# Kernel tuning notes

Hardware: AMD Instinct MI355X
Metric: run time of the kernel (lower is better)

Reference implementation:

```python
import math
import jax, jax.numpy as jnp
import numpy as np

NUM_HEADS = 32
NUM_KV_HEADS = 8
HEAD_SIZE = 128
FEATURE_DIM = 64
SEQ_LEN = 2048
WINDOW_SIZE = 64
EPS = 1e-12
MASK_VALUE = -100000000.0


def _make_masks(n: int, w: int):
    # block-diagonal ones(w,w) tiles, plus the rolled (sub-diagonal) tiles
    m = math.ceil(n / w)
    mask = np.kron(np.eye(m), np.ones((w, w)))
    mask = mask + np.roll(mask, -w, axis=-1)
    mask = mask[:n, :n]
    mask_window = np.tril(mask).astype(bool)[None, None]          # [1,1,n,n]
    mask_linear = np.tril(1.0 - mask).astype(bool)[None, None]    # [1,1,n,n]
    return jnp.asarray(mask_window), jnp.asarray(mask_linear)


def _feature_map(w, x):
    # f(x) = clamp(cat(softmax(xW), softmax(-xW)), min=eps)
    z = jnp.einsum('hdf,bhld->bhlf', w, x)
    return jnp.clip(
        jnp.concatenate([jax.nn.softmax(z, axis=-1), jax.nn.softmax(-z, axis=-1)], axis=-1),
        EPS, None)


def setup_inputs() -> dict:
    key = jax.random.key(0)
    ks = jax.random.split(key, 6)
    return {
        'query': jax.random.normal(ks[0], (SEQ_LEN, NUM_HEADS * HEAD_SIZE), dtype=jnp.float32),
        'key': jax.random.normal(ks[1], (SEQ_LEN, NUM_KV_HEADS * HEAD_SIZE), dtype=jnp.float32),
        'value': jax.random.normal(ks[2], (SEQ_LEN, NUM_KV_HEADS * HEAD_SIZE), dtype=jnp.float32),
        'fmap_q_w': 0.02 * jax.random.normal(ks[3], (NUM_HEADS, HEAD_SIZE, FEATURE_DIM), dtype=jnp.float32),
        'fmap_k_w': 0.02 * jax.random.normal(ks[4], (NUM_HEADS, HEAD_SIZE, FEATURE_DIM), dtype=jnp.float32),
        'window_factors': jax.random.normal(ks[5], (1, NUM_HEADS, 1, 1), dtype=jnp.float32),
    }


def reference(query, key, value, fmap_q_w, fmap_k_w, window_factors):
    T = query.shape[0]
    q = query.reshape(T, NUM_HEADS, HEAD_SIZE)
    k = key.reshape(T, NUM_KV_HEADS, HEAD_SIZE)
    v = value.reshape(T, NUM_KV_HEADS, HEAD_SIZE)
    rep = NUM_HEADS // NUM_KV_HEADS
    k = jnp.repeat(k, rep, axis=1)
    v = jnp.repeat(v, rep, axis=1)
    # [T,H,D] -> [1,H,T,D]
    q = jnp.moveaxis(q, 0, -2)[None]
    k = jnp.moveaxis(k, 0, -2)[None]
    v = jnp.moveaxis(v, 0, -2)[None]

    f_q = _feature_map(fmap_q_w, q)  # [1,H,T,2F]
    f_k = _feature_map(fmap_k_w, k)
    wf = jax.nn.sigmoid(window_factors)

    mask_window, mask_linear = _make_masks(SEQ_LEN, WINDOW_SIZE)
    mask_window = mask_window[:, :, :T, :T]
    mask_linear = mask_linear[:, :, :T, :T]

    # sliding-window softmax term
    a_sm = jnp.einsum('bhmd,bhnd->bhmn', q, k) * (HEAD_SIZE ** -0.5)
    a_sm = jnp.where(mask_window, a_sm, MASK_VALUE)
    a_sm_max = jnp.max(a_sm, axis=-1, keepdims=True)
    a_sm = wf * jnp.exp(a_sm - a_sm_max)
    sum_sm = jnp.sum(a_sm, axis=-1, keepdims=True)

    # linear feature-map term (linear_factor = 1)
    a_ln = jnp.einsum('bhmd,bhnd->bhmn', f_q, f_k)
    a_ln = jnp.where(mask_linear, a_ln, 0.0)
    sum_ln = jnp.sum(a_ln, axis=-1, keepdims=True)

    y = jnp.einsum('bhmn,bhnd->bhmd', a_sm + a_ln, v)
    return y / (sum_sm + sum_ln)
```

## Files before the change

### kernel.cpp

```cpp
#include <hip/hip_runtime.h>
#include <math.h>

#define T_SEQ 2048
#define NH    32
#define NKV   8
#define HS    128
#define FD    64
#define NBLK  32
#define SCAN_NB 30
#define EPSF  1e-12f
#define LDP   136
#define STP   129

typedef unsigned short u16;
typedef __bf16 bf16x8 __attribute__((ext_vector_type(8)));
typedef float  f32x4  __attribute__((ext_vector_type(4)));

__device__ __forceinline__ u16 f2b(float f) {
  unsigned u = __builtin_bit_cast(unsigned, f);
  return (u16)((u + 0x7fffu + ((u >> 16) & 1u)) >> 16);
}

#define FKT_OFF 0
#define ST_OFF  16777216
#define VT_OFF  54525952
#define WT_OFF  58720256
#define KB_OFF  59768832

__global__ __launch_bounds__(256) void k_pre(
    const float* __restrict__ wq, const float* __restrict__ wk,
    const float* __restrict__ vg,
    u16* __restrict__ WT, u16* __restrict__ VT)
{
  __shared__ float sB[128 * 68];
  const int bx = blockIdx.x, tid = threadIdx.x;

  if (bx < 64) {
    const int h = bx >> 1, isk = bx & 1;
    const float* src = (isk ? wk : wq) + (size_t)h * HS * FD;
    for (int idx = tid * 4; idx < 8192; idx += 1024) {
      int r = idx >> 6, c = idx & 63;
      *(float4*)(sB + r * 68 + c) = *(const float4*)(src + idx);
    }
    __syncthreads();
    u16* dst = WT + ((size_t)(isk * NH + h)) * 8192;
    for (int i = 0; i < 8; ++i) {
      int ch = tid + i * 256;
      int f = ch >> 5, d4 = (ch & 31) * 4;
      ushort4 u;
      u.x = f2b(sB[(d4 + 0) * 68 + f]);
      u.y = f2b(sB[(d4 + 1) * 68 + f]);
      u.z = f2b(sB[(d4 + 2) * 68 + f]);
      u.w = f2b(sB[(d4 + 3) * 68 + f]);
      *(ushort4*)(dst + f * 128 + d4) = u;
    }
  } else {
    const int idx2 = bx - 64;
    const int b = idx2 & 31, kvh = idx2 >> 5;
    float* sV = sB;
    for (int idx = tid * 4; idx < 8192; idx += 1024) {
      int r = idx >> 7, c = idx & 127;
      *(float4*)(sV + r * 129 + c) = *(const float4*)(vg + (size_t)(b * 64 + r) * (NKV * HS) + kvh * HS + c);
    }
    __syncthreads();
    const int lane = tid & 63, w = tid >> 6;
#pragma unroll
    for (int i = 0; i < 32; ++i) {
      int d = w * 32 + i;
      VT[((size_t)(kvh * 128 + d)) * T_SEQ + b * 64 + lane] = f2b(sV[lane * 129 + d]);
    }
  }
}

__global__ __launch_bounds__(256) void k_fmap(
    const float* __restrict__ kg, const u16* __restrict__ WT,
    u16* __restrict__ FKT, u16* __restrict__ KBB)
{
  __shared__ __align__(16) u16 smem[2 * 64 * 136];
  u16* sX = smem;
  u16* sW = smem + 64 * 136;
  const int lt = blockIdx.x, h = blockIdx.y;
  const int tid = threadIdx.x, lane = tid & 63, w = tid >> 6;
  const int quad = lane >> 4, txn = lane & 15;

  const float* xbase = kg + (h >> 2) * HS;
  const int    xstr  = NKV * HS;
  for (int idx = tid * 4; idx < 8192; idx += 1024) {
    int r = idx >> 7, c = idx & 127;
    float4 v4 = *(const float4*)(xbase + (size_t)(lt * 64 + r) * xstr + c);
    ushort4 u; u.x = f2b(v4.x); u.y = f2b(v4.y); u.z = f2b(v4.z); u.w = f2b(v4.w);
    *(ushort4*)(sX + r * 136 + c) = u;
  }
  const u16* wt = WT + ((size_t)(NH + h)) * 8192;
  for (int i = 0; i < 4; ++i) {
    int ch = tid + i * 256;
    int row = ch >> 4, d8 = (ch & 15) * 8;
    *(uint4*)(sW + row * 136 + d8) = *(const uint4*)(wt + row * 128 + d8);
  }
  __syncthreads();

  if ((h & 3) == 0) {
    u16* ob = KBB + ((size_t)((h >> 2) * NBLK + lt)) * 8192;
    for (int i = 0; i < 4; ++i) {
      int ch = tid + i * 256;
      int row = ch >> 4, d8 = (ch & 15) * 8;
      *(uint4*)(ob + row * 128 + d8) = *(const uint4*)(sX + row * 136 + d8);
    }
  }

  const int arow = w * 16 + txn;
  const f32x4 vzero = {0.f, 0.f, 0.f, 0.f};
  f32x4 zt[4] = {vzero, vzero, vzero, vzero};
#pragma unroll
  for (int ks = 0; ks < 4; ++ks) {
    bf16x8 a = *(const bf16x8*)(sX + arow * 136 + ks * 32 + quad * 8);
#pragma unroll
    for (int nt = 0; nt < 4; ++nt) {
      bf16x8 bb = *(const bf16x8*)(sW + (nt * 16 + txn) * 136 + ks * 32 + quad * 8);
      zt[nt] = __builtin_amdgcn_mfma_f32_16x16x32_bf16(a, bb, zt[nt], 0, 0, 0);
    }
  }

  float E1[4][4], E2[4][4];
#pragma unroll
  for (int r = 0; r < 4; ++r) {
    float zv[4];
    float mx = -1e30f, mn = 1e30f;
#pragma unroll
    for (int nt = 0; nt < 4; ++nt) {
      zv[nt] = zt[nt][r];
      mx = fmaxf(mx, zv[nt]); mn = fminf(mn, zv[nt]);
    }
#pragma unroll
    for (int o = 1; o < 16; o <<= 1) {
      mx = fmaxf(mx, __shfl_xor(mx, o));
      mn = fminf(mn, __shfl_xor(mn, o));
    }
    float e1[4], e2[4], s1 = 0.f, s2 = 0.f;
#pragma unroll
    for (int nt = 0; nt < 4; ++nt) {
      e1[nt] = __expf(zv[nt] - mx); s1 += e1[nt];
      e2[nt] = __expf(mn - zv[nt]); s2 += e2[nt];
    }
#pragma unroll
    for (int o = 1; o < 16; o <<= 1) { s1 += __shfl_xor(s1, o); s2 += __shfl_xor(s2, o); }
    float r1 = 1.f / s1, r2 = 1.f / s2;
#pragma unroll
    for (int nt = 0; nt < 4; ++nt) {
      E1[r][nt] = fmaxf(e1[nt] * r1, EPSF);
      E2[r][nt] = fmaxf(e2[nt] * r2, EPSF);
    }
  }

  __syncthreads();

#pragma unroll
  for (int r = 0; r < 4; ++r) {
    int j = w * 16 + quad * 4 + r;
#pragma unroll
    for (int nt = 0; nt < 4; ++nt) {
      sX[(nt * 16 + txn) * 68 + j]        = f2b(E1[r][nt]);
      sX[(nt * 16 + txn + 64) * 68 + j]   = f2b(E2[r][nt]);
    }
  }
  __syncthreads();
  u16* ob = FKT + (size_t)h * 128 * T_SEQ + lt * 64;
  for (int i = 0; i < 8; ++i) {
    int ch = tid + i * 256;
    int row = ch >> 4, j4 = (ch & 15) * 4;
    *(ushort4*)(ob + (size_t)row * T_SEQ + j4) = *(const ushort4*)(sX + row * 68 + j4);
  }
}

__global__ __launch_bounds__(256) void k_scan(
    const u16* __restrict__ FKT, const u16* __restrict__ VT, u16* __restrict__ ST)
{
  __shared__ __align__(16) u16 sVT[16 * 72];
  __shared__ __align__(16) u16 sFK[64 * 72];
  const int L = blockIdx.x + 8 * blockIdx.y + 16 * blockIdx.z;
  const int xcd = L & 7, j = L >> 3;
  const int hsub = j & 3, fh = (j >> 2) & 1, dc = j >> 3;
  const int h = xcd * 4 + hsub;
  const int tid = threadIdx.x, lane = tid & 63, w = tid >> 6;
  const int quad = lane >> 4, txn = lane & 15;
  const bool doz = (dc == 0);

  bf16x8 vone;
#pragma unroll
  for (int jj = 0; jj < 8; ++jj) vone[jj] = (__bf16)1.0f;

  const u16* vbase = VT + ((size_t)((h >> 2) * 128 + dc * 16)) * T_SEQ;
  const u16* fbase = FKT + ((size_t)(h * 128 + fh * 64)) * T_SEQ;

  const int srow = tid >> 4, sj4 = (tid & 15) * 4;
  ushort4 rv, rf[4];
  rv = *(const ushort4*)(vbase + (size_t)srow * T_SEQ + sj4);
#pragma unroll
  for (int i = 0; i < 4; ++i) {
    int ch = tid + i * 256;
    int fr = ch >> 4, fj4 = (ch & 15) * 4;
    rf[i] = *(const ushort4*)(fbase + (size_t)fr * T_SEQ + fj4);
  }

  const f32x4 vzero = {0.f, 0.f, 0.f, 0.f};
  f32x4 acc = vzero, zacc = vzero;

  for (int b = 0; b < SCAN_NB; ++b) {
    __syncthreads();
    *(ushort4*)(sVT + srow * 72 + sj4) = rv;
#pragma unroll
    for (int i = 0; i < 4; ++i) {
      int ch = tid + i * 256;
      int fr = ch >> 4, fj4 = (ch & 15) * 4;
      *(ushort4*)(sFK + fr * 72 + fj4) = rf[i];
    }
    __syncthreads();
    if (b + 1 < SCAN_NB) {
      rv = *(const ushort4*)(vbase + (size_t)srow * T_SEQ + (b + 1) * 64 + sj4);
#pragma unroll
      for (int i = 0; i < 4; ++i) {
        int ch = tid + i * 256;
        int fr = ch >> 4, fj4 = (ch & 15) * 4;
        rf[i] = *(const ushort4*)(fbase + (size_t)fr * T_SEQ + (b + 1) * 64 + fj4);
      }
    }
#pragma unroll
    for (int ks = 0; ks < 2; ++ks) {
      bf16x8 a  = *(const bf16x8*)(sVT + txn * 72 + ks * 32 + quad * 8);
      bf16x8 bb = *(const bf16x8*)(sFK + (w * 16 + txn) * 72 + ks * 32 + quad * 8);
      acc = __builtin_amdgcn_mfma_f32_16x16x32_bf16(a, bb, acc, 0, 0, 0);
      if (doz) zacc = __builtin_amdgcn_mfma_f32_16x16x32_bf16(vone, bb, zacc, 0, 0, 0);
    }
    u16* Sb = ST + (((size_t)(h * NBLK + b)) * STP + dc * 16) * 128 + fh * 64;
#pragma unroll
    for (int r = 0; r < 4; ++r)
      Sb[(quad * 4 + r) * 128 + w * 16 + txn] = f2b(acc[r]);
    if (doz && quad == 0)
      ST[(((size_t)(h * NBLK + b)) * STP + 128) * 128 + fh * 64 + w * 16 + txn] = f2b(zacc[0]);
  }
}

__global__ __launch_bounds__(512, 6) void k_main(
    const float* __restrict__ qg, const u16* __restrict__ KBB,
    const u16* __restrict__ WT, const u16* __restrict__ ST,
    const u16* __restrict__ VT, const float* __restrict__ wfac,
    float* __restrict__ out)
{
  __shared__ __align__(16) u16 RA[64 * LDP];
  __shared__ __align__(16) u16 RB[64 * LDP];
  __shared__ __align__(16) u16 sz[128];
  __shared__ float sred[256];
  const int L = blockIdx.x + 32 * blockIdx.y;
  const int xcd = L & 7, jj = L >> 3;
  const int hsub = jj & 3, B = jj >> 2;
  const int h = xcd * 4 + hsub;
  const int tid = threadIdx.x;
  const int lane = tid & 63, w = tid >> 6;
  const int wq_ = w & 3, wt = w >> 2;
  const int quad = lane >> 4, txn = lane & 15;
  const int arow = wq_ * 16 + txn;
  const int koff = quad * 8;

  const f32x4 vzero = {0.f, 0.f, 0.f, 0.f};
  f32x4 y[4];
#pragma unroll
  for (int t = 0; t < 4; ++t) y[t] = vzero;
  float sln[4] = {0.f, 0.f, 0.f, 0.f};
  const bf16x8 bzero = {0, 0, 0, 0, 0, 0, 0, 0};

  const int kb0 = (B >= 1) ? B - 1 : 0;
  const u16* ktB = KBB + ((size_t)((h >> 2) * NBLK + B)) * 8192;
  const u16* ktP = KBB + ((size_t)((h >> 2) * NBLK + kb0)) * 8192;
  const u16* vts = VT  + (size_t)((h >> 2) * 128) * T_SEQ;
  const u16* wqt = WT  + (size_t)h * 8192;
  const u16* ssrc = ST + ((size_t)(h * NBLK + (B >= 2 ? B - 2 : 0))) * (STP * 128);

  auto stage_full = [&](const u16* __restrict__ src) {
#pragma unroll
    for (int i = 0; i < 2; ++i) {
      int idx = tid * 8 + i * 4096, rr = idx >> 7, c = idx & 127;
      *(uint4*)(RB + rr * LDP + c) = *(const uint4*)(src + idx);
    }
  };
  auto stage_qk = [&](int p) {
#pragma unroll
    for (int i = 0; i < 2; ++i) {
      int idx = tid * 8 + i * 4096, rr = idx >> 7, c = idx & 127;
      const u16* src = (rr < 32) ? (ktB + (p * 32 + rr) * 128)
                                 : (ktP + (p * 32 + rr - 32) * 128);
      *(uint4*)(RB + rr * LDP + c) = *(const uint4*)(src + c);
    }
  };
  auto stage_v = [&](int p) {
#pragma unroll
    for (int i = 0; i < 2; ++i) {
      int idx = tid * 8 + i * 4096, rr = idx >> 7, c = idx & 127;
      int d = (rr < 32) ? (p * 32 + rr) : (64 + p * 32 + rr - 32);
      int key = (c < 64) ? (kb0 * 64 + c) : (B * 64 + (c - 64));
      *(uint4*)(RB + rr * LDP + c) = *(const uint4*)(vts + (size_t)d * T_SEQ + key);
    }
  };
  auto stage_s = [&](int p) {
#pragma unroll
    for (int i = 0; i < 2; ++i) {
      int idx = tid * 8 + i * 4096, rr = idx >> 7, c = idx & 127;
      int d = (rr < 32) ? (p * 32 + rr) : (64 + p * 32 + rr - 32);
      *(uint4*)(RB + rr * LDP + c) = *(const uint4*)(ssrc + d * 128 + c);
    }
  };

#pragma unroll
  for (int i = 0; i < 4; ++i) {
    int idx = tid * 4 + i * 2048;
    int r = idx >> 7, c = idx & 127;
    float4 v4 = *(const float4*)(qg + (size_t)(B * 64 + r) * (NH * HS) + h * HS + c);
    ushort4 u; u.x = f2b(v4.x); u.y = f2b(v4.y); u.z = f2b(v4.z); u.w = f2b(v4.w);
    *(ushort4*)(RA + r * LDP + c) = u;
  }
  if (B >= 2) stage_full(wqt);
  __syncthreads();

  f32x4 zt[4] = {vzero, vzero, vzero, vzero};
  if (B >= 2) {
#pragma unroll
    for (int ks = 0; ks < 4; ++ks) {
      bf16x8 a = *(const bf16x8*)(RA + arow * LDP + ks * 32 + koff);
#pragma unroll
      for (int nt = 0; nt < 4; ++nt) {
        bf16x8 bb = *(const bf16x8*)(RB + (nt * 16 + txn) * LDP + ks * 32 + koff);
        zt[nt] = __builtin_amdgcn_mfma_f32_16x16x32_bf16(a, bb, zt[nt], 0, 0, 0);
      }
    }
  }
  __syncthreads();
  stage_qk(0);

  unsigned Epk[4][4];
  if (B >= 2) {
#pragma unroll
    for (int r = 0; r < 4; ++r) {
      float zv[4];
      float mx = -1e30f, mn = 1e30f;
#pragma unroll
      for (int nt = 0; nt < 4; ++nt) {
        zv[nt] = zt[nt][r];
        mx = fmaxf(mx, zv[nt]); mn = fminf(mn, zv[nt]);
      }
#pragma unroll
      for (int o = 1; o < 16; o <<= 1) {
        mx = fmaxf(mx, __shfl_xor(mx, o));
        mn = fminf(mn, __shfl_xor(mn, o));
      }
      float e1[4], e2[4], s1 = 0.f, s2 = 0.f;
#pragma unroll
      for (int nt = 0; nt < 4; ++nt) {
        e1[nt] = __expf(zv[nt] - mx); s1 += e1[nt];
        e2[nt] = __expf(mn - zv[nt]); s2 += e2[nt];
      }
#pragma unroll
      for (int o = 1; o < 16; o <<= 1) { s1 += __shfl_xor(s1, o); s2 += __shfl_xor(s2, o); }
      float r1 = 1.f / s1, r2 = 1.f / s2;
#pragma unroll
      for (int nt = 0; nt < 4; ++nt) {
        unsigned lo = f2b(fmaxf(e1[nt] * r1, EPSF));
        unsigned hi = f2b(fmaxf(e2[nt] * r2, EPSF));
        Epk[r][nt] = lo | (hi << 16);
      }
    }
  }
  __syncthreads();

  f32x4 s[4];
#pragma unroll
  for (int t = 0; t < 4; ++t) s[t] = vzero;
#pragma unroll
  for (int ks = 0; ks < 4; ++ks) {
    bf16x8 a = *(const bf16x8*)(RA + arow * LDP + ks * 32 + koff);
#pragma unroll
    for (int tl = 0; tl < 2; ++tl) {
      if (wt == 0 && B == 0) continue;
      int row = (wt ? 0 : 32) + tl * 16 + txn;
      bf16x8 bb = *(const bf16x8*)(RB + row * LDP + ks * 32 + koff);
      s[tl] = __builtin_amdgcn_mfma_f32_16x16x32_bf16(a, bb, s[tl], 0, 0, 0);
    }
  }
  __syncthreads();
  stage_qk(1);
  __syncthreads();
#pragma unroll
  for (int ks = 0; ks < 4; ++ks) {
    bf16x8 a = *(const bf16x8*)(RA + arow * LDP + ks * 32 + koff);
#pragma unroll
    for (int tl = 0; tl < 2; ++tl) {
      if (wt == 0 && B == 0) continue;
      int row = (wt ? 0 : 32) + tl * 16 + txn;
      bf16x8 bb = *(const bf16x8*)(RB + row * LDP + ks * 32 + koff);
      s[2 + tl] = __builtin_amdgcn_mfma_f32_16x16x32_bf16(a, bb, s[2 + tl], 0, 0, 0);
    }
  }

  float wf = wfac[h];
  wf = 1.f / (1.f + __expf(-wf));
  const float scale = 0.08838834764831845f;
  float mh[4];
#pragma unroll
  for (int r = 0; r < 4; ++r) {
    const int irow = wq_ * 16 + quad * 4 + r;
    float m = -1e30f;
#pragma unroll
    for (int sl = 0; sl < 4; ++sl) {
      float x = s[sl][r] * scale;
      bool msk = wt ? (sl * 16 + txn > irow) : (B == 0);
      x = msk ? -1e30f : x;
      s[sl][r] = x;
      m = fmaxf(m, x);
    }
#pragma unroll
    for (int o = 1; o < 16; o <<= 1) m = fmaxf(m, __shfl_xor(m, o));
    mh[r] = m;
  }
  if (txn == 0) {
#pragma unroll
    for (int r = 0; r < 4; ++r) sred[wt * 64 + wq_ * 16 + quad * 4 + r] = mh[r];
  }
  __syncthreads();

  float ssum[4];
#pragma unroll
  for (int r = 0; r < 4; ++r) {
    const int irow = wq_ * 16 + quad * 4 + r;
    float m = fmaxf(mh[r], sred[(wt ^ 1) * 64 + wq_ * 16 + quad * 4 + r]);
    float ss = 0.f;
#pragma unroll
    for (int sl = 0; sl < 4; ++sl) {
      float e = (s[sl][r] > -1e29f) ? wf * __expf(s[sl][r] - m) : 0.f;
      ss += e;
      RA[irow * LDP + wt * 64 + sl * 16 + txn] = f2b(e);
    }
#pragma unroll
    for (int o = 1; o < 16; o <<= 1) ss += __shfl_xor(ss, o);
    ssum[r] = ss;
  }
  if (txn == 0) {
#pragma unroll
    for (int r = 0; r < 4; ++r) sred[128 + wt * 64 + wq_ * 16 + quad * 4 + r] = ssum[r];
  }
  stage_v(0);
  __syncthreads();
#pragma unroll
  for (int r = 0; r < 4; ++r)
    ssum[r] += sred[128 + (wt ^ 1) * 64 + wq_ * 16 + quad * 4 + r];

#pragma unroll
  for (int ks = 0; ks < 4; ++ks) {
    if (B == 0 && ks < 2) continue;
    bf16x8 a = *(const bf16x8*)(RA + arow * LDP + ks * 32 + koff);
#pragma unroll
    for (int tl = 0; tl < 2; ++tl) {
      int row = wt * 32 + tl * 16 + txn;
      bf16x8 bb = *(const bf16x8*)(RB + row * LDP + ks * 32 + koff);
      y[tl] = __builtin_amdgcn_mfma_f32_16x16x32_bf16(a, bb, y[tl], 0, 0, 0);
    }
  }
  __syncthreads();
  stage_v(1);
  __syncthreads();
#pragma unroll
  for (int ks = 0; ks < 4; ++ks) {
    if (B == 0 && ks < 2) continue;
    bf16x8 a = *(const bf16x8*)(RA + arow * LDP + ks * 32 + koff);
#pragma unroll
    for (int tl = 0; tl < 2; ++tl) {
      int row = wt * 32 + tl * 16 + txn;
      bf16x8 bb = *(const bf16x8*)(RB + row * LDP + ks * 32 + koff);
      y[2 + tl] = __builtin_amdgcn_mfma_f32_16x16x32_bf16(a, bb, y[2 + tl], 0, 0, 0);
    }
  }
  __syncthreads();

  if (B >= 2) {
#pragma unroll
    for (int r = 0; r < 4; ++r) {
      int row = wq_ * 16 + quad * 4 + r;
#pragma unroll
      for (int nt = 0; nt < 4; ++nt) {
        u16 val = wt ? (u16)(Epk[r][nt] >> 16) : (u16)(Epk[r][nt] & 0xffffu);
        RA[row * LDP + wt * 64 + nt * 16 + txn] = val;
      }
    }
  }
  stage_s(0);
  if (tid < 32) *(ushort4*)(sz + tid * 4) = *(const ushort4*)(ssrc + 16384 + tid * 4);
  __syncthreads();

  f32x4 yz = vzero;
  if (B >= 2) {
#pragma unroll
    for (int ks = 0; ks < 4; ++ks) {
      bf16x8 a = *(const bf16x8*)(RA + arow * LDP + ks * 32 + koff);
#pragma unroll
      for (int tl = 0; tl < 2; ++tl) {
        int row = wt * 32 + tl * 16 + txn;
        bf16x8 bb = *(const bf16x8*)(RB + row * LDP + ks * 32 + koff);
        y[tl] = __builtin_amdgcn_mfma_f32_16x16x32_bf16(a, bb, y[tl], 0, 0, 0);
      }
      bf16x8 bz = (txn == 0) ? *(const bf16x8*)(sz + ks * 32 + koff) : bzero;
      yz = __builtin_amdgcn_mfma_f32_16x16x32_bf16(a, bz, yz, 0, 0, 0);
    }
  }
  __syncthreads();
  stage_s(1);
  __syncthreads();
  if (B >= 2) {
#pragma unroll
    for (int ks = 0; ks < 4; ++ks) {
      bf16x8 a = *(const bf16x8*)(RA + arow * LDP + ks * 32 + koff);
#pragma unroll
      for (int tl = 0; tl < 2; ++tl) {
        int row = wt * 32 + tl * 16 + txn;
        bf16x8 bb = *(const bf16x8*)(RB + row * LDP + ks * 32 + koff);
        y[2 + tl] = __builtin_amdgcn_mfma_f32_16x16x32_bf16(a, bb, y[2 + tl], 0, 0, 0);
      }
    }
#pragma unroll
    for (int r = 0; r < 4; ++r) sln[r] = __shfl(yz[r], lane & 48);
  }

  const size_t obase = ((size_t)h * T_SEQ + B * 64) * HS;
#pragma unroll
  for (int r = 0; r < 4; ++r) {
    float inv = 1.f / (ssum[r] + sln[r]);
    int irow = wq_ * 16 + quad * 4 + r;
#pragma unroll
    for (int yl = 0; yl < 4; ++yl) {
      int t = wt * 4 + yl;
      out[obase + (size_t)irow * HS + t * 16 + txn] = y[yl][r] * inv;
    }
  }
}

extern "C" void kernel_launch(void* const* d_in, const int* in_sizes, int n_in,
                              void* d_out, int out_size, void* d_ws, size_t ws_size,
                              hipStream_t stream) {
  const float* q    = (const float*)d_in[0];
  const float* k    = (const float*)d_in[1];
  const float* v    = (const float*)d_in[2];
  const float* wq   = (const float*)d_in[3];
  const float* wk   = (const float*)d_in[4];
  const float* wfac = (const float*)d_in[5];
  float* out = (float*)d_out;
  char* wsb = (char*)d_ws;

  u16* FKT = (u16*)(wsb + FKT_OFF);
  u16* ST  = (u16*)(wsb + ST_OFF);
  u16* VT  = (u16*)(wsb + VT_OFF);
  u16* WT  = (u16*)(wsb + WT_OFF);
  u16* KBB = (u16*)(wsb + KB_OFF);

  k_pre  <<<dim3(320),      256, 0, stream>>>(wq, wk, v, WT, VT);
  k_fmap <<<dim3(NBLK, NH), 256, 0, stream>>>(k, WT, FKT, KBB);
  k_scan <<<dim3(8, 2, NH), 256, 0, stream>>>(FKT, VT, ST);
  k_main <<<dim3(NBLK, NH), 512, 0, stream>>>(q, KBB, WT, ST, VT, wfac, out);
}
```

Measured before the change: 163.2 us.

## Double-buffer shared staging in scan and main kernels to cut barriers

Both kernels now stage global tiles into two alternating shared-memory buffers. In k_scan this removes one barrier per iteration. In k_main the next tile (QK, V, S) is staged into the other buffer while MFMAs read the current one, which removes several barrier pairs. The cost is more LDS per block (k_main gains about 17 KB), which may lower occupancy below the requested 6 blocks per CU. The new buffer-reuse pattern also has to be race-free across the remaining barriers.

```diff
diff --git a/kernel.cpp b/kernel.cpp
--- a/kernel.cpp
+++ b/kernel.cpp
@@ -175,8 +175,8 @@
 __global__ __launch_bounds__(256) void k_scan(
     const u16* __restrict__ FKT, const u16* __restrict__ VT, u16* __restrict__ ST)
 {
-  __shared__ __align__(16) u16 sVT[16 * 72];
-  __shared__ __align__(16) u16 sFK[64 * 72];
+  __shared__ __align__(16) u16 sVT[2][16 * 72];
+  __shared__ __align__(16) u16 sFK[2][64 * 72];
   const int L = blockIdx.x + 8 * blockIdx.y + 16 * blockIdx.z;
   const int xcd = L & 7, j = L >> 3;
   const int hsub = j & 3, fh = (j >> 2) & 1, dc = j >> 3;
@@ -204,15 +204,17 @@
 
   const f32x4 vzero = {0.f, 0.f, 0.f, 0.f};
   f32x4 acc = vzero, zacc = vzero;
+  int cur = 0;
 
   for (int b = 0; b < SCAN_NB; ++b) {
-    __syncthreads();
-    *(ushort4*)(sVT + srow * 72 + sj4) = rv;
+    u16* dV = sVT[cur];
+    u16* dF = sFK[cur];
+    *(ushort4*)(dV + srow * 72 + sj4) = rv;
 #pragma unroll
     for (int i = 0; i < 4; ++i) {
       int ch = tid + i * 256;
       int fr = ch >> 4, fj4 = (ch & 15) * 4;
-      *(ushort4*)(sFK + fr * 72 + fj4) = rf[i];
+      *(ushort4*)(dF + fr * 72 + fj4) = rf[i];
     }
     __syncthreads();
     if (b + 1 < SCAN_NB) {
@@ -226,8 +228,8 @@
     }
 #pragma unroll
     for (int ks = 0; ks < 2; ++ks) {
-      bf16x8 a  = *(const bf16x8*)(sVT + txn * 72 + ks * 32 + quad * 8);
-      bf16x8 bb = *(const bf16x8*)(sFK + (w * 16 + txn) * 72 + ks * 32 + quad * 8);
+      bf16x8 a  = *(const bf16x8*)(dV + txn * 72 + ks * 32 + quad * 8);
+      bf16x8 bb = *(const bf16x8*)(dF + (w * 16 + txn) * 72 + ks * 32 + quad * 8);
       acc = __builtin_amdgcn_mfma_f32_16x16x32_bf16(a, bb, acc, 0, 0, 0);
       if (doz) zacc = __builtin_amdgcn_mfma_f32_16x16x32_bf16(vone, bb, zacc, 0, 0, 0);
     }
@@ -237,6 +239,7 @@
       Sb[(quad * 4 + r) * 128 + w * 16 + txn] = f2b(acc[r]);
     if (doz && quad == 0)
       ST[(((size_t)(h * NBLK + b)) * STP + 128) * 128 + fh * 64 + w * 16 + txn] = f2b(zacc[0]);
+    cur ^= 1;
   }
 }
 
@@ -247,9 +250,10 @@
     float* __restrict__ out)
 {
   __shared__ __align__(16) u16 RA[64 * LDP];
-  __shared__ __align__(16) u16 RB[64 * LDP];
+  __shared__ __align__(16) u16 RB0[64 * LDP];
+  __shared__ __align__(16) u16 RB1[64 * LDP];
   __shared__ __align__(16) u16 sz[128];
-  __shared__ float sred[256];
+  __shared__ float sred[128];
   const int L = blockIdx.x + 32 * blockIdx.y;
   const int xcd = L & 7, jj = L >> 3;
   const int hsub = jj & 3, B = jj >> 2;
@@ -275,37 +279,37 @@
   const u16* wqt = WT  + (size_t)h * 8192;
   const u16* ssrc = ST + ((size_t)(h * NBLK + (B >= 2 ? B - 2 : 0))) * (STP * 128);
 
-  auto stage_full = [&](const u16* __restrict__ src) {
+  auto stage_full = [&](u16* dst, const u16* __restrict__ src) {
 #pragma unroll
     for (int i = 0; i < 2; ++i) {
       int idx = tid * 8 + i * 4096, rr = idx >> 7, c = idx & 127;
-      *(uint4*)(RB + rr * LDP + c) = *(const uint4*)(src + idx);
+      *(uint4*)(dst + rr * LDP + c) = *(const uint4*)(src + idx);
     }
   };
-  auto stage_qk = [&](int p) {
+  auto stage_qk = [&](u16* dst, int p) {
 #pragma unroll
     for (int i = 0; i < 2; ++i) {
       int idx = tid * 8 + i * 4096, rr = idx >> 7, c = idx & 127;
       const u16* src = (rr < 32) ? (ktB + (p * 32 + rr) * 128)
                                  : (ktP + (p * 32 + rr - 32) * 128);
-      *(uint4*)(RB + rr * LDP + c) = *(const uint4*)(src + c);
+      *(uint4*)(dst + rr * LDP + c) = *(const uint4*)(src + c);
     }
   };
-  auto stage_v = [&](int p) {
+  auto stage_v = [&](u16* dst, int p) {
 #pragma unroll
     for (int i = 0; i < 2; ++i) {
       int idx = tid * 8 + i * 4096, rr = idx >> 7, c = idx & 127;
       int d = (rr < 32) ? (p * 32 + rr) : (64 + p * 32 + rr - 32);
       int key = (c < 64) ? (kb0 * 64 + c) : (B * 64 + (c - 64));
-      *(uint4*)(RB + rr * LDP + c) = *(const uint4*)(vts + (size_t)d * T_SEQ + key);
+      *(uint4*)(dst + rr * LDP + c) = *(const uint4*)(vts + (size_t)d * T_SEQ + key);
     }
   };
-  auto stage_s = [&](int p) {
+  auto stage_s = [&](u16* dst, int p) {
 #pragma unroll
     for (int i = 0; i < 2; ++i) {
       int idx = tid * 8 + i * 4096, rr = idx >> 7, c = idx & 127;
       int d = (rr < 32) ? (p * 32 + rr) : (64 + p * 32 + rr - 32);
-      *(uint4*)(RB + rr * LDP + c) = *(const uint4*)(ssrc + d * 128 + c);
+      *(uint4*)(dst + rr * LDP + c) = *(const uint4*)(ssrc + d * 128 + c);
     }
   };
 
@@ -317,7 +321,8 @@
     ushort4 u; u.x = f2b(v4.x); u.y = f2b(v4.y); u.z = f2b(v4.z); u.w = f2b(v4.w);
     *(ushort4*)(RA + r * LDP + c) = u;
   }
-  if (B >= 2) stage_full(wqt);
+  if (B >= 2) stage_full(RB0, wqt);
+  stage_qk(RB1, 0);
   __syncthreads();
 
   f32x4 zt[4] = {vzero, vzero, vzero, vzero};
@@ -327,14 +332,29 @@
       bf16x8 a = *(const bf16x8*)(RA + arow * LDP + ks * 32 + koff);
 #pragma unroll
       for (int nt = 0; nt < 4; ++nt) {
-        bf16x8 bb = *(const bf16x8*)(RB + (nt * 16 + txn) * LDP + ks * 32 + koff);
+        bf16x8 bb = *(const bf16x8*)(RB0 + (nt * 16 + txn) * LDP + ks * 32 + koff);
         zt[nt] = __builtin_amdgcn_mfma_f32_16x16x32_bf16(a, bb, zt[nt], 0, 0, 0);
       }
     }
   }
-  __syncthreads();
-  stage_qk(0);
-
+  f32x4 s[4];
+#pragma unroll
+  for (int t = 0; t < 4; ++t) s[t] = vzero;
+#pragma unroll
+  for (int ks = 0; ks < 4; ++ks) {
+    bf16x8 a = *(const bf16x8*)(RA + arow * LDP + ks * 32 + koff);
+#pragma unroll
+    for (int tl = 0; tl < 2; ++tl) {
+      if (wt == 0 && B == 0) continue;
+      int row = (wt ? 0 : 32) + tl * 16 + txn;
+      bf16x8 bb = *(const bf16x8*)(RB1 + row * LDP + ks * 32 + koff);
+      s[tl] = __builtin_amdgcn_mfma_f32_16x16x32_bf16(a, bb, s[tl], 0, 0, 0);
+    }
+  }
+  __syncthreads();
+
+  stage_qk(RB0, 1);
+  stage_v(RB1, 0);
   unsigned Epk[4][4];
   if (B >= 2) {
 #pragma unroll
@@ -370,9 +390,6 @@
   }
   __syncthreads();
 
-  f32x4 s[4];
-#pragma unroll
-  for (int t = 0; t < 4; ++t) s[t] = vzero;
 #pragma unroll
   for (int ks = 0; ks < 4; ++ks) {
     bf16x8 a = *(const bf16x8*)(RA + arow * LDP + ks * 32 + koff);
@@ -380,25 +397,10 @@
     for (int tl = 0; tl < 2; ++tl) {
       if (wt == 0 && B == 0) continue;
       int row = (wt ? 0 : 32) + tl * 16 + txn;
-      bf16x8 bb = *(const bf16x8*)(RB + row * LDP + ks * 32 + koff);
-      s[tl] = __builtin_amdgcn_mfma_f32_16x16x32_bf16(a, bb, s[tl], 0, 0, 0);
-    }
-  }
-  __syncthreads();
-  stage_qk(1);
-  __syncthreads();
-#pragma unroll
-  for (int ks = 0; ks < 4; ++ks) {
-    bf16x8 a = *(const bf16x8*)(RA + arow * LDP + ks * 32 + koff);
-#pragma unroll
-    for (int tl = 0; tl < 2; ++tl) {
-      if (wt == 0 && B == 0) continue;
-      int row = (wt ? 0 : 32) + tl * 16 + txn;
-      bf16x8 bb = *(const bf16x8*)(RB + row * LDP + ks * 32 + koff);
+      bf16x8 bb = *(const bf16x8*)(RB0 + row * LDP + ks * 32 + koff);
       s[2 + tl] = __builtin_amdgcn_mfma_f32_16x16x32_bf16(a, bb, s[2 + tl], 0, 0, 0);
     }
   }
-
   float wf = wfac[h];
   wf = 1.f / (1.f + __expf(-wf));
   const float scale = 0.08838834764831845f;
@@ -425,6 +427,7 @@
   }
   __syncthreads();
 
+  stage_v(RB0, 1);
   float ssum[4];
 #pragma unroll
   for (int r = 0; r < 4; ++r) {
@@ -443,14 +446,13 @@
   }
   if (txn == 0) {
 #pragma unroll
-    for (int r = 0; r < 4; ++r) sred[128 + wt * 64 + wq_ * 16 + quad * 4 + r] = ssum[r];
-  }
-  stage_v(0);
-  __syncthreads();
+    for (int r = 0; r < 4; ++r) sred[(wt ^ 1) * 64 + wq_ * 16 + quad * 4 + r] = ssum[r];
+  }
+  __syncthreads();
+
 #pragma unroll
   for (int r = 0; r < 4; ++r)
-    ssum[r] += sred[128 + (wt ^ 1) * 64 + wq_ * 16 + quad * 4 + r];
-
+    ssum[r] += sred[wt * 64 + wq_ * 16 + quad * 4 + r];
 #pragma unroll
   for (int ks = 0; ks < 4; ++ks) {
     if (B == 0 && ks < 2) continue;
@@ -458,13 +460,14 @@
 #pragma unroll
     for (int tl = 0; tl < 2; ++tl) {
       int row = wt * 32 + tl * 16 + txn;
-      bf16x8 bb = *(const bf16x8*)(RB + row * LDP + ks * 32 + koff);
+      bf16x8 bb = *(const bf16x8*)(RB1 + row * LDP + ks * 32 + koff);
       y[tl] = __builtin_amdgcn_mfma_f32_16x16x32_bf16(a, bb, y[tl], 0, 0, 0);
     }
   }
   __syncthreads();
-  stage_v(1);
-  __syncthreads();
+
+  stage_s(RB1, 0);
+  if (tid < 32) *(ushort4*)(sz + tid * 4) = *(const ushort4*)(ssrc + 16384 + tid * 4);
 #pragma unroll
   for (int ks = 0; ks < 4; ++ks) {
     if (B == 0 && ks < 2) continue;
@@ -472,7 +475,7 @@
 #pragma unroll
     for (int tl = 0; tl < 2; ++tl) {
       int row = wt * 32 + tl * 16 + txn;
-      bf16x8 bb = *(const bf16x8*)(RB + row * LDP + ks * 32 + koff);
+      bf16x8 bb = *(const bf16x8*)(RB0 + row * LDP + ks * 32 + koff);
       y[2 + tl] = __builtin_amdgcn_mfma_f32_16x16x32_bf16(a, bb, y[2 + tl], 0, 0, 0);
     }
   }
@@ -489,8 +492,7 @@
       }
     }
   }
-  stage_s(0);
-  if (tid < 32) *(ushort4*)(sz + tid * 4) = *(const ushort4*)(ssrc + 16384 + tid * 4);
+  stage_s(RB0, 1);
   __syncthreads();
 
   f32x4 yz = vzero;
@@ -501,24 +503,19 @@
 #pragma unroll
       for (int tl = 0; tl < 2; ++tl) {
         int row = wt * 32 + tl * 16 + txn;
-        bf16x8 bb = *(const bf16x8*)(RB + row * LDP + ks * 32 + koff);
+        bf16x8 bb = *(const bf16x8*)(RB1 + row * LDP + ks * 32 + koff);
         y[tl] = __builtin_amdgcn_mfma_f32_16x16x32_bf16(a, bb, y[tl], 0, 0, 0);
       }
       bf16x8 bz = (txn == 0) ? *(const bf16x8*)(sz + ks * 32 + koff) : bzero;
       yz = __builtin_amdgcn_mfma_f32_16x16x32_bf16(a, bz, yz, 0, 0, 0);
     }
-  }
-  __syncthreads();
-  stage_s(1);
-  __syncthreads();
-  if (B >= 2) {
 #pragma unroll
     for (int ks = 0; ks < 4; ++ks) {
       bf16x8 a = *(const bf16x8*)(RA + arow * LDP + ks * 32 + koff);
 #pragma unroll
       for (int tl = 0; tl < 2; ++tl) {
         int row = wt * 32 + tl * 16 + txn;
-        bf16x8 bb = *(const bf16x8*)(RB + row * LDP + ks * 32 + koff);
+        bf16x8 bb = *(const bf16x8*)(RB0 + row * LDP + ks * 32 + koff);
         y[2 + tl] = __builtin_amdgcn_mfma_f32_16x16x32_bf16(a, bb, y[2 + tl], 0, 0, 0);
       }
     }
```

After: 168.7 us. 3.4% more time.
